# Kernel optimization log

Hardware: AMD Instinct MI355X
Metric: run time of the kernel (lower is better)

Reference implementation:

```python
import jax, jax.numpy as jnp
import numpy as np

EMBED_DIM = 1024
NUM_HEADS = 16
MICRO_HEADS = 8
HEAD_DIM = EMBED_DIM // NUM_HEADS
N_BLOCKS = NUM_HEADS // MICRO_HEADS
B, N = 2, 2048


def setup_inputs() -> dict:
    key = jax.random.key(0)
    ks = jax.random.split(key, 9)
    s = 1.0 / np.sqrt(EMBED_DIM)
    return {
        "x": jax.random.normal(ks[0], (B, N, EMBED_DIM), dtype=jnp.float32),
        "Wq": jax.random.uniform(ks[1], (EMBED_DIM, EMBED_DIM), jnp.float32, -s, s),
        "bq": jax.random.uniform(ks[2], (EMBED_DIM,), jnp.float32, -s, s),
        "Wk": jax.random.uniform(ks[3], (EMBED_DIM, EMBED_DIM), jnp.float32, -s, s),
        "bk": jax.random.uniform(ks[4], (EMBED_DIM,), jnp.float32, -s, s),
        "Wv": jax.random.uniform(ks[5], (EMBED_DIM, EMBED_DIM), jnp.float32, -s, s),
        "bv": jax.random.uniform(ks[6], (EMBED_DIM,), jnp.float32, -s, s),
        "Wo": jax.random.uniform(ks[7], (EMBED_DIM, EMBED_DIM), jnp.float32, -s, s),
        "bo": jax.random.uniform(ks[8], (EMBED_DIM,), jnp.float32, -s, s),
    }


def _scramble(t, b, n):
    # Replicates torch's Qh[:, :, hs:he, :].contiguous().view(B*mh, N, dh)
    # which is a raw row-major reshape mixing (N, mh) -> (mh, N) per batch.
    # (B, N, E) -> (B, N, nb, mh, dh) -> (B, nb, N, mh, dh) -> raw reshape -> (B, nb, mh, N, dh)
    t = t.reshape(b, n, N_BLOCKS, MICRO_HEADS, HEAD_DIM)
    t = jnp.transpose(t, (0, 2, 1, 3, 4))
    return t.reshape(b, N_BLOCKS, MICRO_HEADS, n, HEAD_DIM)


def reference(x, Wq, bq, Wk, bk, Wv, bv, Wo, bo):
    b, n, e = x.shape
    scale = HEAD_DIM ** -0.5
    Q = x @ Wq.T + bq
    K = x @ Wk.T + bk
    V = x @ Wv.T + bv
    q = _scramble(Q, b, n)  # (B, nb, mh, N, dh)
    k = _scramble(K, b, n)
    v = _scramble(V, b, n)
    s = jnp.einsum("bgmqd,bgmkd->bgmqk", q, k) * scale  # (B, nb, mh, N, N)
    causal = jnp.tril(jnp.ones((n, n), dtype=bool))
    s = jnp.where(causal, s, -jnp.inf)
    p = jax.nn.softmax(s, axis=-1)
    ctx = jnp.einsum("bgmqk,bgmkd->bgmqd", p, v)  # (B, nb, mh, N, dh)
    # inverse raw reshape: (mh, N, dh) -> (N, mh*dh) per (b, g), then concat blocks
    ctx = ctx.reshape(b, N_BLOCKS, n, MICRO_HEADS * HEAD_DIM)
    ctx = jnp.transpose(ctx, (0, 2, 1, 3)).reshape(b, n, e)
    return ctx @ Wo.T + bo
```

## Files before the change

kernel.cpp:

```cpp
#include <hip/hip_runtime.h>
#include <hip/hip_bf16.h>


typedef unsigned short ushortT;
typedef __attribute__((ext_vector_type(8))) short short8;
typedef __attribute__((ext_vector_type(4))) float floatx4;

__device__ inline float bf2f(ushortT u) {
    union { unsigned int i; float f; } v; v.i = ((unsigned int)u) << 16; return v.f;
}
__device__ inline ushortT f2bf(float f) {
    union { float f; unsigned int i; } v; v.f = f;
    unsigned int x = v.i;
    return (ushortT)((x + 0x7fffu + ((x >> 16) & 1u)) >> 16);
}

__device__ inline void gl_lds16(const ushortT* g, ushortT* lds) {
    __builtin_amdgcn_global_load_lds(
        (const __attribute__((address_space(1))) unsigned int*)g,
        (__attribute__((address_space(3))) unsigned int*)lds, 16, 0, 0);
}

__global__ __launch_bounds__(256) void cvt_bf16(
    const float* __restrict__ x,
    const float* __restrict__ Wq, const float* __restrict__ Wk,
    const float* __restrict__ Wv, const float* __restrict__ Wo,
    ushortT* __restrict__ xb, ushortT* __restrict__ Wb)
{
    const unsigned tid = blockIdx.x * 256 + threadIdx.x;
    const size_t e = (size_t)tid * 8;
    const float* src;
    ushortT* dst;
    size_t off;
    if (e < (size_t)(4u << 20)) { src = x; dst = xb; off = e; }
    else {
        const size_t r = e - (size_t)(4u << 20);
        const int wsel = (int)(r >> 20);
        off = r & 0xFFFFFu;
        src = (wsel == 0) ? Wq : (wsel == 1) ? Wk : (wsel == 2) ? Wv : Wo;
        dst = Wb + ((size_t)wsel << 20);
    }
    const float4 f0 = ((const float4*)(src + off))[0];
    const float4 f1 = ((const float4*)(src + off))[1];
    union { __hip_bfloat162 h[4]; uint4 u; } pk;
    pk.h[0] = __float22bfloat162_rn(float2{f0.x, f0.y});
    pk.h[1] = __float22bfloat162_rn(float2{f0.z, f0.w});
    pk.h[2] = __float22bfloat162_rn(float2{f1.x, f1.y});
    pk.h[3] = __float22bfloat162_rn(float2{f1.z, f1.w});
    *(uint4*)(dst + off) = pk.u;
}

template <bool OUT_F32, bool N64>
__global__ __launch_bounds__(256) void gemm_lds(
    const ushortT* __restrict__ A, const ushortT* __restrict__ Wst,
    const float* __restrict__ b0, const float* __restrict__ b1, const float* __restrict__ b2,
    void* __restrict__ O0, void* __restrict__ O1, void* __restrict__ O2)
{
    constexpr int NT = N64 ? 64 : 128;
    constexpr int NJ = N64 ? 2 : 4;
    constexpr int WQ = N64 ? 2 : 4;
    __shared__ __align__(16) ushortT As[128 * 64];
    __shared__ __align__(16) ushortT Bs[NT * 64];
    const int t = threadIdx.x;
    const int m0 = blockIdx.y * 128;
    const int n0g = blockIdx.x * NT;
    const int mat = n0g >> 10;
    const int n0 = n0g & 1023;
    const ushortT* W = Wst + ((size_t)mat << 20);
    const float* bias = (mat == 0) ? b0 : (mat == 1) ? b1 : b2;
    void* Out        = (mat == 0) ? O0 : (mat == 1) ? O1 : O2;

    const int w = t >> 6, lane = t & 63;
    const int wm = w >> 1, wn = w & 1;
    const int col16 = lane & 15, quad = lane >> 4;

    floatx4 acc[4][NJ];
    for (int i = 0; i < 4; i++)
        for (int j = 0; j < NJ; j++) acc[i][j] = (floatx4)0.0f;

    const int cid0 = w * (N64 ? 128 : 256) + lane;

    for (int k0 = 0; k0 < 1024; k0 += 64) {
        #pragma unroll
        for (int q = 0; q < 4; q++) {
            const int cid = w * 256 + q * 64 + lane;
            const int row = cid >> 3;
            const int sch = (cid & 7) ^ (row & 7);
            gl_lds16(A + (size_t)(m0 + row) * 1024 + k0 + sch * 8,
                     As + (size_t)(w * 256 + q * 64) * 8);
        }
        #pragma unroll
        for (int q = 0; q < WQ; q++) {
            const int cid = cid0 + q * 64;
            const int row = cid >> 3;
            const int sch = (cid & 7) ^ (row & 7);
            gl_lds16(W + (size_t)(n0 + row) * 1024 + k0 + sch * 8,
                     Bs + (size_t)(w * (N64 ? 128 : 256) + q * 64) * 8);
        }
        __syncthreads();
        #pragma unroll
        for (int ks = 0; ks < 64; ks += 32) {
            const int cbase = (ks >> 3) + quad;
            const int sw = col16 & 7;
            short8 a[4], b[NJ];
            #pragma unroll
            for (int i = 0; i < 4; i++) {
                const int row = wm * 64 + i * 16 + col16;
                a[i] = *(const short8*)(As + row * 64 + ((cbase ^ sw) << 3));
            }
            #pragma unroll
            for (int j = 0; j < NJ; j++) {
                const int row = wn * (NT / 2) + j * 16 + col16;
                b[j] = *(const short8*)(Bs + row * 64 + ((cbase ^ sw) << 3));
            }
            #pragma unroll
            for (int i = 0; i < 4; i++)
                #pragma unroll
                for (int j = 0; j < NJ; j++)
                    acc[i][j] = __builtin_amdgcn_mfma_f32_16x16x32_bf16(b[j], a[i], acc[i][j], 0, 0, 0);
        }
        __syncthreads();
    }

    #pragma unroll
    for (int i = 0; i < 4; i++) {
        const int m = m0 + wm * 64 + i * 16 + col16;
        #pragma unroll
        for (int j = 0; j < NJ; j++) {
            const int nb = n0 + wn * (NT / 2) + j * 16 + quad * 4;
            const float4 bv4 = *(const float4*)(bias + nb);
            const float v0 = acc[i][j][0] + bv4.x;
            const float v1 = acc[i][j][1] + bv4.y;
            const float v2 = acc[i][j][2] + bv4.z;
            const float v3 = acc[i][j][3] + bv4.w;
            if constexpr (OUT_F32) {
                *(float4*)((float*)Out + (size_t)m * 1024 + nb) = float4{v0, v1, v2, v3};
            } else {
                union { __hip_bfloat162 h[2]; unsigned long long u; } pk2;
                pk2.h[0] = __float22bfloat162_rn(float2{v0, v1});
                pk2.h[1] = __float22bfloat162_rn(float2{v2, v3});
                *(unsigned long long*)((ushortT*)Out + (size_t)m * 1024 + nb) = pk2.u;
            }
        }
    }
}

__global__ __launch_bounds__(256) void transpose_v(
    const ushortT* __restrict__ Vb, ushortT* __restrict__ VT)
{
    __shared__ ushortT L[64 * 65];
    const int bid = blockIdx.x;
    const int pt = bid & 31, s = bid >> 5;
    const int bb = s >> 4, g = (s >> 3) & 1, mh = s & 7;
    const size_t baseoff = (size_t)bb * 2048 * 1024 + (size_t)g * 512;
    const int t = threadIdx.x;
    {
        const int pr = t >> 2, seg = t & 3;
        const int i = mh * 2048 + pt * 64 + pr;
        const uint4* src = (const uint4*)(Vb + baseoff + (size_t)(i >> 3) * 1024 + (i & 7) * 64 + seg * 16);
        union { uint4 u[2]; ushortT h[16]; } tmp;
        tmp.u[0] = src[0]; tmp.u[1] = src[1];
        #pragma unroll
        for (int d = 0; d < 16; d++) L[pr * 65 + seg * 16 + d] = tmp.h[d];
    }
    __syncthreads();
    {
        const int dc = t >> 2, pseg = t & 3;
        union { uint4 u[2]; ushortT h[16]; } tmp;
        #pragma unroll
        for (int j = 0; j < 16; j++) tmp.h[j] = L[(pseg * 16 + j) * 65 + dc];
        uint4* dst = (uint4*)(VT + (size_t)s * 64 * 2048 + (size_t)dc * 2048 + pt * 64 + pseg * 16);
        dst[0] = tmp.u[0]; dst[1] = tmp.u[1];
    }
}

__global__ __launch_bounds__(256) void attn(
    const ushortT* __restrict__ Qb, const ushortT* __restrict__ Kb,
    const ushortT* __restrict__ VT, ushortT* __restrict__ Cb)
{
    __shared__ __align__(16) ushortT lds[20480];

    const int t = threadIdx.x;
    const int bid = blockIdx.x;
    const int xcd = bid & 7;
    const int u = bid >> 3;
    const int s = xcd * 4 + (u & 3);
    const int x5 = u >> 2;
    const int qt = (x5 < 8) ? x5 : (x5 < 16) ? (39 - x5)
                 : (x5 < 24) ? (x5 - 8) : (47 - x5);
    const int bb = s >> 4, g = (s >> 3) & 1, mh = s & 7;

    const int w = t >> 6, lane = t & 63;
    const int col16 = lane & 15, quad = lane >> 4;

    const size_t baseoff = (size_t)bb * 2048 * 1024 + (size_t)g * 512;
    const size_t vtbase  = (size_t)s * 64 * 2048;
    const int i0 = mh * 2048 + qt * 64;
    const int qloc = w * 16 + col16;
    const int c7 = col16 & 7;
    const float KL = 0.125f * 1.44269504f;

    short8 qreg[2];
    {
        const int i = i0 + qloc;
        const ushortT* p = Qb + baseoff + (size_t)(i >> 3) * 1024 + (i & 7) * 64;
        qreg[0] = *(const short8*)(p + quad * 8);
        qreg[1] = *(const short8*)(p + 32 + quad * 8);
    }

    int kbo[2];
    kbo[0] = col16 * 64 + (((0 + quad) ^ c7) << 3);
    kbo[1] = col16 * 64 + (((4 + quad) ^ c7) << 3);
    const int pso0 = 16384 + qloc * 64 + (((0 + quad) ^ c7) << 3);
    const int pso1 = 16384 + qloc * 64 + (((4 + quad) ^ c7) << 3);
    int pwo[4];
    #pragma unroll
    for (int c = 0; c < 4; c++) {
        const int key0 = c * 16 + quad * 4;
        pwo[c] = 16384 + qloc * 64 + ((((key0 >> 3) ^ c7)) << 3) + (key0 & 7);
    }

    const int cid0 = w * 128 + lane, cid1 = cid0 + 64;
    const int row0 = cid0 >> 3, sch0 = (cid0 & 7) ^ (row0 & 7);
    const int row1 = cid1 >> 3, sch1 = (cid1 & 7) ^ (row1 & 7);
    const int jr0 = mh * 2048 + row0;
    const int jr1 = mh * 2048 + row1;
    const ushortT* gk0 = Kb + baseoff + (size_t)(jr0 >> 3) * 1024 + (jr0 & 7) * 64 + sch0 * 8;
    const ushortT* gk1 = Kb + baseoff + (size_t)(jr1 >> 3) * 1024 + (jr1 & 7) * 64 + sch1 * 8;
    const ushortT* gv0 = VT + vtbase + (size_t)row0 * 2048 + sch0 * 8;
    const ushortT* gv1 = VT + vtbase + (size_t)row1 * 2048 + sch1 * 8;
    const int sdK = w * 1024;

    auto stage = [&](int sb) {
        gl_lds16(gk0, lds + sb + sdK);
        gl_lds16(gk1, lds + sb + sdK + 512);
        gl_lds16(gv0, lds + sb + 8192 + sdK);
        gl_lds16(gv1, lds + sb + 8192 + sdK + 512);
        gk0 += 8192; gk1 += 8192; gv0 += 64; gv1 += 64;
    };

    float l_s = 0.f;
    floatx4 Oacc[4];
    for (int c = 0; c < 4; c++) Oacc[c] = (floatx4)0.0f;

    stage(0);
    int sb = 4096;
    for (int kt = 0; kt <= qt; ++kt) {
        __syncthreads();
        if (kt < qt) { stage(sb); sb ^= 4096; }

        floatx4 sc[4];
        for (int c = 0; c < 4; c++) sc[c] = (floatx4)0.0f;
        #pragma unroll
        for (int h = 0; h < 2; h++) {
            const short8 bq = qreg[h];
            #pragma unroll
            for (int c = 0; c < 4; c++) {
                const short8 ak = *(const short8*)(lds + kbo[h] + c * 1024);
                sc[c] = __builtin_amdgcn_mfma_f32_16x16x32_bf16(ak, bq, sc[c], 0, 0, 0);
            }
        }

        if (kt == qt) {
            #pragma unroll
            for (int c = 0; c < 4; c++)
                #pragma unroll
                for (int r = 0; r < 4; r++)
                    if ((c * 16 + quad * 4 + r) > qloc) sc[c][r] = -1e30f;
        }

        float lsum = l_s;
        #pragma unroll
        for (int c = 0; c < 4; c++) {
            #pragma unroll
            for (int r = 0; r < 4; r++) {
                const float pv = exp2f(sc[c][r] * KL);
                sc[c][r] = pv;
                lsum += pv;
            }
            union { __hip_bfloat162 h[2]; unsigned long long u; } pk2;
            pk2.h[0] = __float22bfloat162_rn(float2{sc[c][0], sc[c][1]});
            pk2.h[1] = __float22bfloat162_rn(float2{sc[c][2], sc[c][3]});
            *(unsigned long long*)(lds + pwo[c]) = pk2.u;
        }
        l_s = lsum;

        #pragma unroll
        for (int h = 0; h < 2; h++) {
            const short8 bp = *(const short8*)(lds + (h ? pso1 : pso0));
            #pragma unroll
            for (int c = 0; c < 4; c++) {
                const short8 av = *(const short8*)(lds + kbo[h] + 8192 + c * 1024);
                Oacc[c] = __builtin_amdgcn_mfma_f32_16x16x32_bf16(av, bp, Oacc[c], 0, 0, 0);
            }
        }

        kbo[0] ^= 4096; kbo[1] ^= 4096;
    }

    l_s += __shfl_xor(l_s, 16);
    l_s += __shfl_xor(l_s, 32);

    {
        const int i = i0 + qloc;
        const float inv = 1.0f / l_s;
        ushortT* dst = Cb + baseoff + (size_t)(i >> 3) * 1024 + (i & 7) * 64;
        #pragma unroll
        for (int c = 0; c < 4; c++) {
            union { __hip_bfloat162 h[2]; unsigned long long u; } pk2;
            pk2.h[0] = __float22bfloat162_rn(float2{Oacc[c][0] * inv, Oacc[c][1] * inv});
            pk2.h[1] = __float22bfloat162_rn(float2{Oacc[c][2] * inv, Oacc[c][3] * inv});
            *(unsigned long long*)(dst + c * 16 + quad * 4) = pk2.u;
        }
    }
}

extern "C" void kernel_launch(void* const* d_in, const int* in_sizes, int n_in,
                              void* d_out, int out_size, void* d_ws, size_t ws_size,
                              hipStream_t stream)
{
    const float* x  = (const float*)d_in[0];
    const float* Wq = (const float*)d_in[1];
    const float* bq = (const float*)d_in[2];
    const float* Wk = (const float*)d_in[3];
    const float* bk = (const float*)d_in[4];
    const float* Wv = (const float*)d_in[5];
    const float* bv = (const float*)d_in[6];
    const float* Wo = (const float*)d_in[7];
    const float* bo = (const float*)d_in[8];

    const size_t M1 = (size_t)1024 * 1024;
    ushortT* Wb  = (ushortT*)d_ws;
    ushortT* xb  = Wb + 4 * M1;
    ushortT* Qb  = xb + 4 * M1;
    ushortT* Kb  = Qb + 4 * M1;
    ushortT* Vb  = (ushortT*)d_out;
    ushortT* VTb = xb;
    ushortT* Cb  = Qb;

    dim3 blk(256);
    cvt_bf16<<<dim3(4096), blk, 0, stream>>>(x, Wq, Wk, Wv, Wo, xb, Wb);
    gemm_lds<false, false><<<dim3(24, 32), blk, 0, stream>>>(
        xb, Wb, bq, bk, bv, Qb, Kb, Vb);
    transpose_v<<<dim3(1024), blk, 0, stream>>>(Vb, VTb);
    attn<<<dim3(1024), blk, 0, stream>>>(Qb, Kb, VTb, Cb);
    gemm_lds<true, true><<<dim3(16, 32), blk, 0, stream>>>(
        Cb, Wb + 3 * M1, bo, bo, bo, d_out, d_out, d_out);
}
```

Before: 198.1 us.

## Add 256x256-tile 8-wave QKV GEMM with double-buffered direct-to-LDS loads

Replaces the 128x128-tile QKV projection GEMM with a new kernel using 512 threads and 256x256 output tiles. Tiles are double-buffered in 128KB of LDS, filled by global_load_lds with an XOR swizzle and explicit vmcnt waits so loads overlap MFMA work. Blocks are remapped so neighbouring blocks share tiles, and s_setprio is raised around the MFMA bursts. The larger tile cuts global traffic per FLOP, but it yields only 192 workgroups and uses heavy register and LDS footprint, which limits occupancy.

```diff
diff --git a/kernel.cpp b/kernel.cpp
--- a/kernel.cpp
+++ b/kernel.cpp
@@ -48,6 +48,128 @@
     pk.h[2] = __float22bfloat162_rn(float2{f1.x, f1.y});
     pk.h[3] = __float22bfloat162_rn(float2{f1.z, f1.w});
     *(uint4*)(dst + off) = pk.u;
+}
+
+__global__ __launch_bounds__(512, 2) void gemm_qkv_8p(
+    const ushortT* __restrict__ A, const ushortT* __restrict__ Wst,
+    const float* __restrict__ b0, const float* __restrict__ b1, const float* __restrict__ b2,
+    ushortT* __restrict__ O0, ushortT* __restrict__ O1, ushortT* __restrict__ O2)
+{
+    __shared__ __align__(16) ushortT sm[65536];
+
+    const int t = threadIdx.x;
+    const int bid = blockIdx.x;
+    const int wg = (bid & 7) * 24 + (bid >> 3);
+    const int mt = wg / 12;
+    const int nt = wg - mt * 12;
+    const int m0 = mt * 256;
+    const int mat = nt >> 2;
+    const int n0 = (nt & 3) * 256;
+    const ushortT* W = Wst + ((size_t)mat << 20);
+    const float* bias = (mat == 0) ? b0 : (mat == 1) ? b1 : b2;
+    ushortT* Out     = (mat == 0) ? O0 : (mat == 1) ? O1 : O2;
+
+    const int w = t >> 6, lane = t & 63;
+    const int wm = w >> 2, wn = w & 3;
+    const int col16 = lane & 15, quad = lane >> 4;
+    const int c7 = col16 & 7;
+
+    const int ko[2] = { ((0 + quad) ^ c7) << 3, ((4 + quad) ^ c7) << 3 };
+    const int xbase = (wm * 128 + col16) * 64;
+    const int wbase = (wn * 64 + col16) * 64;
+
+    const int trow = t >> 3;
+    const int sch = (t & 7) ^ (trow & 7);
+    const ushortT* gA[4]; const ushortT* gB[4];
+    #pragma unroll
+    for (int q = 0; q < 4; q++) {
+        gA[q] = A + (size_t)(m0 + q * 64 + trow) * 1024 + sch * 8;
+        gB[q] = W + (size_t)(n0 + q * 64 + trow) * 1024 + sch * 8;
+    }
+    const int dst0 = (w << 6) * 8;
+
+    floatx4 acc[8][4];
+    #pragma unroll
+    for (int i = 0; i < 8; i++)
+        #pragma unroll
+        for (int j = 0; j < 4; j++) acc[i][j] = (floatx4)0.0f;
+
+    auto issue8 = [&](const int ab, const int bb) {
+        #pragma unroll
+        for (int q = 0; q < 4; q++) {
+            gl_lds16(gA[q], sm + ab + dst0 + q * 4096);
+            gl_lds16(gB[q], sm + bb + dst0 + q * 4096);
+            gA[q] += 64; gB[q] += 64;
+        }
+    };
+
+    auto group = [&](const int ab, const int bb) {
+        short8 bw[4];
+        #pragma unroll
+        for (int ks = 0; ks < 2; ks++) {
+            #pragma unroll
+            for (int mh = 0; mh < 2; mh++) {
+                short8 bx[4];
+                if (mh == 0) {
+                    #pragma unroll
+                    for (int nf = 0; nf < 4; nf++)
+                        bw[nf] = *(const short8*)(sm + bb + wbase + nf * 1024 + ko[ks]);
+                }
+                #pragma unroll
+                for (int j = 0; j < 4; j++)
+                    bx[j] = *(const short8*)(sm + ab + xbase + (mh * 4 + j) * 1024 + ko[ks]);
+                __builtin_amdgcn_s_barrier();
+                __builtin_amdgcn_s_setprio(1);
+                #pragma unroll
+                for (int j = 0; j < 4; j++)
+                    #pragma unroll
+                    for (int nf = 0; nf < 4; nf++)
+                        acc[mh * 4 + j][nf] = __builtin_amdgcn_mfma_f32_16x16x32_bf16(
+                            bw[nf], bx[j], acc[mh * 4 + j][nf], 0, 0, 0);
+                __builtin_amdgcn_s_setprio(0);
+                __builtin_amdgcn_s_barrier();
+            }
+        }
+    };
+
+    issue8(0, 16384);
+    issue8(32768, 49152);
+
+    #pragma unroll 1
+    for (int it = 0; it < 7; ++it) {
+        asm volatile("s_waitcnt vmcnt(8)" ::: "memory");
+        __builtin_amdgcn_s_barrier();
+        group(0, 16384);
+        issue8(0, 16384);
+        asm volatile("s_waitcnt vmcnt(8)" ::: "memory");
+        __builtin_amdgcn_s_barrier();
+        group(32768, 49152);
+        issue8(32768, 49152);
+    }
+    asm volatile("s_waitcnt vmcnt(8)" ::: "memory");
+    __builtin_amdgcn_s_barrier();
+    group(0, 16384);
+    asm volatile("s_waitcnt vmcnt(0)" ::: "memory");
+    __builtin_amdgcn_s_barrier();
+    group(32768, 49152);
+
+    #pragma unroll
+    for (int mf = 0; mf < 8; mf++) {
+        const int m = m0 + wm * 128 + mf * 16 + col16;
+        #pragma unroll
+        for (int nf = 0; nf < 4; nf++) {
+            const int nb = n0 + wn * 64 + nf * 16 + quad * 4;
+            const float4 bv4 = *(const float4*)(bias + nb);
+            const float v0 = acc[mf][nf][0] + bv4.x;
+            const float v1 = acc[mf][nf][1] + bv4.y;
+            const float v2 = acc[mf][nf][2] + bv4.z;
+            const float v3 = acc[mf][nf][3] + bv4.w;
+            union { __hip_bfloat162 h[2]; unsigned long long u; } pk2;
+            pk2.h[0] = __float22bfloat162_rn(float2{v0, v1});
+            pk2.h[1] = __float22bfloat162_rn(float2{v2, v3});
+            *(unsigned long long*)(Out + (size_t)m * 1024 + nb) = pk2.u;
+        }
+    }
 }
 
 template <bool OUT_F32, bool N64>
@@ -340,7 +462,7 @@
 
     dim3 blk(256);
     cvt_bf16<<<dim3(4096), blk, 0, stream>>>(x, Wq, Wk, Wv, Wo, xb, Wb);
-    gemm_lds<false, false><<<dim3(24, 32), blk, 0, stream>>>(
+    gemm_qkv_8p<<<dim3(192), dim3(512), 0, stream>>>(
         xb, Wb, bq, bk, bv, Qb, Kb, Vb);
     transpose_v<<<dim3(1024), blk, 0, stream>>>(Vb, VTb);
     attn<<<dim3(1024), blk, 0, stream>>>(Qb, Kb, VTb, Cb);
```

New measurement: 192.7 us. -2.7%, faster.
